# Kernel optimization log

Measured on AMD Instinct MI355X. Metric: run time of the kernel, lower is better.

Reference implementation:

```python
import jax, jax.numpy as jnp
import numpy as np

B, S, H = 4, 1024, 2048      # batch, seq_len, hidden_size
N, D = 16, 128               # num_attention_heads, attention_head_size (num_kv_heads == N)
W_SCALE = 0.02


def setup_inputs() -> dict:
    key = jax.random.key(0)
    ks = jax.random.split(key, 7)
    hidden_states = jax.random.normal(ks[0], (B, S, H), dtype=jnp.float32)
    # Per-head query projections (stacked over the head axis) + shared K/V projections.
    Wq = jax.random.normal(ks[1], (N, H, D), dtype=jnp.float32) * W_SCALE
    bq = jax.random.normal(ks[2], (N, D), dtype=jnp.float32) * W_SCALE
    Wk = jax.random.normal(ks[3], (H, D), dtype=jnp.float32) * W_SCALE
    bk = jax.random.normal(ks[4], (D,), dtype=jnp.float32) * W_SCALE
    Wv = jax.random.normal(ks[5], (H, D), dtype=jnp.float32) * W_SCALE
    bv = jax.random.normal(ks[6], (D,), dtype=jnp.float32) * W_SCALE
    return {"hidden_states": hidden_states, "Wq": Wq, "bq": bq,
            "Wk": Wk, "bk": bk, "Wv": Wv, "bv": bv}


def reference(hidden_states, Wq, bq, Wk, bk, Wv, bv):
    # Batched equivalent of the per-head Python loop:
    # q_i = Linear_i(h); k = key_layer(h); v = value_layer(h) (shared across heads,
    # repeat_interleave is a no-op since num_kv_heads == num_attention_heads).
    Q = jnp.einsum('bsh,nhd->bnsd', hidden_states, Wq) + bq[None, :, None, :]  # [B,N,S,D]
    K = hidden_states @ Wk + bk   # [B,S,D]
    V = hidden_states @ Wv + bv   # [B,S,D]
    # NOTE: source applies no 1/sqrt(D) scaling.
    scores = jnp.einsum('bnsd,btd->bnst', Q, K)          # [B,N,S,S]
    attn = jax.nn.softmax(scores, axis=-1)
    out = jnp.einsum('bnst,btd->bnsd', attn, V)          # [B,N,S,D]
    return out
```

## Files before the change

kernel.cpp:

```cpp
#include <hip/hip_runtime.h>
#include <hip/hip_bf16.h>

typedef unsigned short ushort_t;
typedef _Float16 half_t;
typedef __attribute__((ext_vector_type(8))) _Float16 h8;
typedef __attribute__((ext_vector_type(8))) short short8;
typedef __attribute__((ext_vector_type(4))) float f32x4;
typedef __attribute__((ext_vector_type(4))) float f4;

#define NB 4
#define SS 1024
#define HH 2048
#define NH 16
#define DD 128
#define MM (NB*SS)
#define NTOT 2304
#define COL_K 2048
#define COL_V 2176
#define KVB 64
#define L2E 1.44269504089f

__device__ __forceinline__ ushort_t f2h(float x) {
    half_t h = (half_t)x;
    return *(ushort_t*)&h;
}
__device__ __forceinline__ f32x4 mfma16h(h8 a, h8 b, f32x4 c) {
    return __builtin_amdgcn_mfma_f32_16x16x32_f16(a, b, c, 0, 0, 0);
}
__device__ __forceinline__ void load_lds16(const ushort_t* g, ushort_t* l) {
    __builtin_amdgcn_global_load_lds(
        (const __attribute__((address_space(1))) unsigned int*)g,
        (__attribute__((address_space(3))) unsigned int*)l,
        16, 0, 0);
}

__global__ void k_cvt(const float* __restrict__ src, ushort_t* __restrict__ dst, int n) {
    int i = (blockIdx.x * blockDim.x + threadIdx.x) * 8;
    if (i + 7 < n) {
        f4 a = *(const f4*)(src + i);
        f4 b = *(const f4*)(src + i + 4);
        short8 o;
        #pragma unroll
        for (int j = 0; j < 4; ++j) { o[j] = (short)f2h(a[j]); o[4 + j] = (short)f2h(b[j]); }
        *(short8*)(dst + i) = o;
    }
}

__global__ __launch_bounds__(256) void k_tw(const float* __restrict__ W,
                                            ushort_t* __restrict__ T, int Dd) {
    __shared__ ushort_t t[64][74];
    const int n = blockIdx.z;
    const int h0 = blockIdx.x * 64, d0 = blockIdx.y * 64;
    const int r = threadIdx.x >> 2, cg = (threadIdx.x & 3) * 16;
    const float* src = W + ((size_t)n * HH + h0 + r) * Dd + d0 + cg;
    #pragma unroll
    for (int v = 0; v < 4; ++v) {
        f4 a = *(const f4*)(src + v * 4);
        #pragma unroll
        for (int j = 0; j < 4; ++j) t[r][cg + v * 4 + j] = f2h(a[j]);
    }
    __syncthreads();
    short8 o0, o1;
    #pragma unroll
    for (int j = 0; j < 8; ++j) { o0[j] = (short)t[cg + j][r]; o1[j] = (short)t[cg + 8 + j][r]; }
    ushort_t* dst = T + ((size_t)(n * Dd + d0 + r)) * HH + h0 + cg;
    *(short8*)dst = o0;
    *(short8*)(dst + 8) = o1;
}

__global__ void k_bias(const float* __restrict__ bq, const float* __restrict__ bk,
                       const float* __restrict__ bv, float* __restrict__ bc) {
    int i = blockIdx.x * 256 + threadIdx.x;
    if (i < NTOT)
        bc[i] = (i < COL_K) ? bq[i] : ((i < COL_V) ? bk[i - COL_K] : bv[i - COL_V]);
}

__global__ __launch_bounds__(256) void k_gemm(
    const ushort_t* __restrict__ A, const ushort_t* __restrict__ B,
    const float* __restrict__ bias, ushort_t* __restrict__ O) {

    constexpr int BK = 32;
    __shared__ ushort_t sA[128 * BK], sB[128 * BK];

    const int bid = blockIdx.x;
    const int swz = (bid & 7) * 72 + (bid >> 3);
    const int m0 = (swz & 31) * 128;
    const int n0 = (swz >> 5) * 128;

    const int tid = threadIdx.x;
    const int w = tid >> 6, l = tid & 63;
    const int wr = w >> 1, wc = w & 1;
    f32x4 acc[4][4] = {};

    for (int kt = 0; kt < HH / BK; ++kt) {
        const int k0 = kt * BK;
        #pragma unroll
        for (int c = 0; c < 2; ++c) {
            int chunk = c * 4 + w;
            int idx = chunk * 512 + l * 8;
            int row = idx >> 5, kc = idx & 31;
            load_lds16(A + (size_t)(m0 + row) * HH + k0 + kc, &sA[chunk * 512]);
            load_lds16(B + (size_t)(n0 + row) * HH + k0 + kc, &sB[chunk * 512]);
        }
        __syncthreads();

        h8 a[4], b[4];
        #pragma unroll
        for (int i = 0; i < 4; ++i) {
            int ra = wr * 64 + i * 16 + (l & 15);
            int rb = wc * 64 + i * 16 + (l & 15);
            a[i] = *(const h8*)&sA[ra * 32 + (l >> 4) * 8];
            b[i] = *(const h8*)&sB[rb * 32 + (l >> 4) * 8];
        }
        #pragma unroll
        for (int i = 0; i < 4; ++i)
            #pragma unroll
            for (int j = 0; j < 4; ++j)
                acc[i][j] = mfma16h(a[i], b[j], acc[i][j]);
        __syncthreads();
    }

    #pragma unroll
    for (int i = 0; i < 4; ++i) {
        int row = m0 + wr * 64 + i * 16 + ((l >> 4) << 2);
        #pragma unroll
        for (int j = 0; j < 4; ++j) {
            int col = n0 + wc * 64 + j * 16 + (l & 15);
            float bv = bias[col];
            #pragma unroll
            for (int r = 0; r < 4; ++r) {
                float cv = acc[i][j][r] + bv;
                O[(size_t)(row + r) * NTOT + col] = f2h(cv);
            }
        }
    }
}

__global__ __launch_bounds__(256) void k_transpose_v(const ushort_t* __restrict__ O,
                                                     ushort_t* __restrict__ Vt) {
    __shared__ ushort_t t[64][74];
    const int tid = threadIdx.x;
    const int bx = blockIdx.x;
    const int by = blockIdx.y;
    int r = tid >> 2, cg = (tid & 3) * 16;
    const ushort_t* src = &O[(size_t)(bx * 64 + r) * NTOT + COL_V + by * 64 + cg];
    short8 v0 = *(const short8*)src;
    short8 v1 = *(const short8*)(src + 8);
    #pragma unroll
    for (int j = 0; j < 8; ++j) { t[r][cg + j] = (ushort_t)v0[j]; t[r][cg + 8 + j] = (ushort_t)v1[j]; }
    __syncthreads();
    short8 o0, o1;
    #pragma unroll
    for (int j = 0; j < 8; ++j) { o0[j] = (short)t[cg + j][r]; o1[j] = (short)t[cg + 8 + j][r]; }
    ushort_t* dst = &Vt[(size_t)(by * 64 + r) * MM + bx * 64 + cg];
    *(short8*)dst = o0;
    *(short8*)(dst + 8) = o1;
}

__global__ __launch_bounds__(512, 4) void k_attn(
    const ushort_t* __restrict__ O, const ushort_t* __restrict__ Vt,
    float* __restrict__ Out) {

    __shared__ ushort_t sK[2][KVB * 128];
    __shared__ ushort_t sVt[2][128 * KVB];

    const int tid = threadIdx.x;
    const int w = tid >> 6, l = tid & 63;
    const int lg = l >> 4, li = l & 15;
    const int q0 = blockIdx.x * 128;
    const int n = blockIdx.y, b = blockIdx.z;

    h8 qv[4];
    {
        size_t base = ((size_t)(b * SS + q0 + w * 16 + li)) * NTOT + n * 128 + lg * 8;
        #pragma unroll
        for (int kk = 0; kk < 4; ++kk)
            qv[kk] = *(const h8*)&O[base + kk * 32];
    }

    f32x4 accO[8] = {};
    float m2 = -3.0e38f;
    float lsum = 0.f;

    auto stage = [&](int bi, int t0) {
        #pragma unroll
        for (int c = 0; c < 2; ++c) {
            int seg = c * 8 + w;
            int oe = seg * 512 + l * 8;
            int row = oe >> 7;
            int mk = (row & 3) | (((row >> 3) & 1) << 2);
            int ce = (oe & 127) ^ (mk << 3);
            size_t g = (size_t)(b * SS + t0 + row) * NTOT + COL_K + ce;
            load_lds16(O + g, &sK[bi][seg * 512]);
        }
        #pragma unroll
        for (int c = 0; c < 2; ++c) {
            int seg = c * 8 + w;
            int oe = seg * 512 + l * 8;
            int row = oe >> 6;
            int ce = (oe & 63) ^ ((row & 7) << 3);
            size_t g = (size_t)row * MM + b * SS + t0 + ce;
            load_lds16(Vt + g, &sVt[bi][seg * 512]);
        }
    };

    stage(0, 0);
    constexpr int NT = SS / KVB;

    for (int it = 0; it < NT; ++it) {
        const int cur = it & 1;
        __syncthreads();
        if (it + 1 < NT) stage(cur ^ 1, (it + 1) * KVB);
        const ushort_t* sKc = sK[cur];
        const ushort_t* sVc = sVt[cur];

        f32x4 s[4] = {};
        #pragma unroll
        for (int ts = 0; ts < 4; ++ts) {
            int trow = (ts & 1) * 32 + ((li >> 2) << 3) + ((ts >> 1) << 2) + (li & 3);
            int mk = (trow & 3) | (((trow >> 3) & 1) << 2);
            #pragma unroll
            for (int kk = 0; kk < 4; ++kk) {
                h8 kv = *(const h8*)&sKc[trow * 128 + ((kk * 32 + lg * 8) ^ (mk << 3))];
                s[ts] = mfma16h(kv, qv[kk], s[ts]);
            }
        }

        float v = fmaxf(fmaxf(s[0][0], s[0][1]), fmaxf(s[0][2], s[0][3]));
        #pragma unroll
        for (int ts = 1; ts < 4; ++ts)
            v = fmaxf(v, fmaxf(fmaxf(s[ts][0], s[ts][1]), fmaxf(s[ts][2], s[ts][3])));
        v = fmaxf(v, __shfl_xor(v, 16));
        v = fmaxf(v, __shfl_xor(v, 32));
        float pm2 = v * L2E;

        if (!__all(pm2 <= m2 + 11.54f)) {
            float mn = fmaxf(m2, pm2);
            float scl = exp2f(m2 - mn);
            lsum *= scl;
            #pragma unroll
            for (int db = 0; db < 8; ++db)
                #pragma unroll
                for (int r = 0; r < 4; ++r) accO[db][r] *= scl;
            m2 = mn;
        }

        h8 pb[2];
        #pragma unroll
        for (int ts = 0; ts < 4; ++ts)
            #pragma unroll
            for (int r = 0; r < 4; ++r) {
                float p = exp2f(fmaf(s[ts][r], L2E, -m2));
                lsum += p;
                pb[ts & 1][((ts >> 1) << 2) + r] = (half_t)p;
            }

        #pragma unroll
        for (int db = 0; db < 8; ++db) {
            int d = db * 16 + li;
            const ushort_t* vbase = &sVc[d * KVB];
            int sw = (d & 7) << 3;
            #pragma unroll
            for (int ks = 0; ks < 2; ++ks) {
                h8 va = *(const h8*)&vbase[(ks * 32 + lg * 8) ^ sw];
                accO[db] = mfma16h(va, pb[ks], accO[db]);
            }
        }
    }

    lsum += __shfl_xor(lsum, 16);
    lsum += __shfl_xor(lsum, 32);
    float inv = 1.0f / lsum;
    int q = q0 + w * 16 + li;
    size_t base = (((size_t)b * NH + n) * SS + q) * DD;
    #pragma unroll
    for (int db = 0; db < 8; ++db) {
        f4 o;
        #pragma unroll
        for (int r = 0; r < 4; ++r) o[r] = accO[db][r] * inv;
        *(f4*)&Out[base + db * 16 + lg * 4] = o;
    }
}

#define OFF_HC    ((size_t)0)
#define OFF_BC    (OFF_HC + (size_t)MM*HH*2)
#define OFF_BIAS  (OFF_BC + (size_t)NTOT*HH*2)
#define OFF_O     (OFF_BIAS + (size_t)16384)
#define OFF_VT    (OFF_O + (size_t)MM*NTOT*2)

extern "C" void kernel_launch(void* const* d_in, const int* in_sizes, int n_in,
                              void* d_out, int out_size, void* d_ws, size_t ws_size,
                              hipStream_t stream) {
    const float* hs = (const float*)d_in[0];
    const float* Wq = (const float*)d_in[1];
    const float* bq = (const float*)d_in[2];
    const float* Wk = (const float*)d_in[3];
    const float* bk = (const float*)d_in[4];
    const float* Wv = (const float*)d_in[5];
    const float* bv = (const float*)d_in[6];
    float* out = (float*)d_out;
    char* ws = (char*)d_ws;

    ushort_t* hc   = (ushort_t*)(ws + OFF_HC);
    ushort_t* bcat = (ushort_t*)(ws + OFF_BC);
    float*    bias = (float*)(ws + OFF_BIAS);
    ushort_t* Obuf = (ushort_t*)(ws + OFF_O);
    ushort_t* vt   = (ushort_t*)(ws + OFF_VT);

    k_cvt<<<(MM*HH)/(256*8), 256, 0, stream>>>(hs, hc, MM*HH);
    dim3 gwq(HH/64, DD/64, NH);
    k_tw<<<gwq, 256, 0, stream>>>(Wq, bcat, DD);
    dim3 gwk(HH/64, DD/64, 1);
    k_tw<<<gwk, 256, 0, stream>>>(Wk, bcat + (size_t)COL_K*HH, DD);
    k_tw<<<gwk, 256, 0, stream>>>(Wv, bcat + (size_t)COL_V*HH, DD);
    k_bias<<<(NTOT + 255)/256, 256, 0, stream>>>(bq, bk, bv, bias);

    k_gemm<<<(MM/128)*(NTOT/128), 256, 0, stream>>>(hc, bcat, bias, Obuf);

    dim3 gt(MM/64, DD/64);
    k_transpose_v<<<gt, 256, 0, stream>>>(Obuf, vt);

    dim3 ga(SS/128, NH, NB);
    k_attn<<<ga, 512, 0, stream>>>(Obuf, vt, out);
}
```

Before: 133.8 us.

## Read V directly from global in attention, drop bias kernel, add setprio

The attention kernel stops staging V^T tiles into shared memory and instead loads V fragments directly from global memory (relying on cache) in the PV MFMA loop, halving LDS use per block. The separate bias concatenation kernel is removed, with the GEMM epilogue selecting bias from bq/bk/bv directly. It also adds s_setprio around MFMA sections. The direct global loads are not prefetched, so their latency may stall the PV loop, in exchange for less LDS traffic and potentially higher occupancy.

```diff
diff --git a/kernel.cpp b/kernel.cpp
--- a/kernel.cpp
+++ b/kernel.cpp
@@ -68,16 +68,10 @@
     *(short8*)(dst + 8) = o1;
 }
 
-__global__ void k_bias(const float* __restrict__ bq, const float* __restrict__ bk,
-                       const float* __restrict__ bv, float* __restrict__ bc) {
-    int i = blockIdx.x * 256 + threadIdx.x;
-    if (i < NTOT)
-        bc[i] = (i < COL_K) ? bq[i] : ((i < COL_V) ? bk[i - COL_K] : bv[i - COL_V]);
-}
-
 __global__ __launch_bounds__(256) void k_gemm(
     const ushort_t* __restrict__ A, const ushort_t* __restrict__ B,
-    const float* __restrict__ bias, ushort_t* __restrict__ O) {
+    const float* __restrict__ bq, const float* __restrict__ bk,
+    const float* __restrict__ bvv, ushort_t* __restrict__ O) {
 
     constexpr int BK = 32;
     __shared__ ushort_t sA[128 * BK], sB[128 * BK];
@@ -126,7 +120,9 @@
         #pragma unroll
         for (int j = 0; j < 4; ++j) {
             int col = n0 + wc * 64 + j * 16 + (l & 15);
-            float bv = bias[col];
+            float bv = (col < COL_K) ? bq[col]
+                     : (col < COL_V) ? bk[col - COL_K]
+                                     : bvv[col - COL_V];
             #pragma unroll
             for (int r = 0; r < 4; ++r) {
                 float cv = acc[i][j][r] + bv;
@@ -162,7 +158,6 @@
     float* __restrict__ Out) {
 
     __shared__ ushort_t sK[2][KVB * 128];
-    __shared__ ushort_t sVt[2][128 * KVB];
 
     const int tid = threadIdx.x;
     const int w = tid >> 6, l = tid & 63;
@@ -193,28 +188,21 @@
             size_t g = (size_t)(b * SS + t0 + row) * NTOT + COL_K + ce;
             load_lds16(O + g, &sK[bi][seg * 512]);
         }
-        #pragma unroll
-        for (int c = 0; c < 2; ++c) {
-            int seg = c * 8 + w;
-            int oe = seg * 512 + l * 8;
-            int row = oe >> 6;
-            int ce = (oe & 63) ^ ((row & 7) << 3);
-            size_t g = (size_t)row * MM + b * SS + t0 + ce;
-            load_lds16(Vt + g, &sVt[bi][seg * 512]);
-        }
     };
 
     stage(0, 0);
     constexpr int NT = SS / KVB;
+    const ushort_t* vtb = Vt + (size_t)b * SS;
 
     for (int it = 0; it < NT; ++it) {
         const int cur = it & 1;
+        const int t0 = it * KVB;
         __syncthreads();
-        if (it + 1 < NT) stage(cur ^ 1, (it + 1) * KVB);
+        if (it + 1 < NT) stage(cur ^ 1, t0 + KVB);
         const ushort_t* sKc = sK[cur];
-        const ushort_t* sVc = sVt[cur];
 
         f32x4 s[4] = {};
+        __builtin_amdgcn_s_setprio(1);
         #pragma unroll
         for (int ts = 0; ts < 4; ++ts) {
             int trow = (ts & 1) * 32 + ((li >> 2) << 3) + ((ts >> 1) << 2) + (li & 3);
@@ -225,6 +213,7 @@
                 s[ts] = mfma16h(kv, qv[kk], s[ts]);
             }
         }
+        __builtin_amdgcn_s_setprio(0);
 
         float v = fmaxf(fmaxf(s[0][0], s[0][1]), fmaxf(s[0][2], s[0][3]));
         #pragma unroll
@@ -255,17 +244,18 @@
                 pb[ts & 1][((ts >> 1) << 2) + r] = (half_t)p;
             }
 
+        __builtin_amdgcn_s_setprio(1);
         #pragma unroll
         for (int db = 0; db < 8; ++db) {
             int d = db * 16 + li;
-            const ushort_t* vbase = &sVc[d * KVB];
-            int sw = (d & 7) << 3;
+            const ushort_t* vrow = vtb + (size_t)d * MM + t0;
             #pragma unroll
             for (int ks = 0; ks < 2; ++ks) {
-                h8 va = *(const h8*)&vbase[(ks * 32 + lg * 8) ^ sw];
+                h8 va = *(const h8*)&vrow[ks * 32 + lg * 8];
                 accO[db] = mfma16h(va, pb[ks], accO[db]);
             }
         }
+        __builtin_amdgcn_s_setprio(0);
     }
 
     lsum += __shfl_xor(lsum, 16);
@@ -284,8 +274,7 @@
 
 #define OFF_HC    ((size_t)0)
 #define OFF_BC    (OFF_HC + (size_t)MM*HH*2)
-#define OFF_BIAS  (OFF_BC + (size_t)NTOT*HH*2)
-#define OFF_O     (OFF_BIAS + (size_t)16384)
+#define OFF_O     (OFF_BC + (size_t)NTOT*HH*2)
 #define OFF_VT    (OFF_O + (size_t)MM*NTOT*2)
 
 extern "C" void kernel_launch(void* const* d_in, const int* in_sizes, int n_in,
@@ -303,7 +292,6 @@
 
     ushort_t* hc   = (ushort_t*)(ws + OFF_HC);
     ushort_t* bcat = (ushort_t*)(ws + OFF_BC);
-    float*    bias = (float*)(ws + OFF_BIAS);
     ushort_t* Obuf = (ushort_t*)(ws + OFF_O);
     ushort_t* vt   = (ushort_t*)(ws + OFF_VT);
 
@@ -313,9 +301,8 @@
     dim3 gwk(HH/64, DD/64, 1);
     k_tw<<<gwk, 256, 0, stream>>>(Wk, bcat + (size_t)COL_K*HH, DD);
     k_tw<<<gwk, 256, 0, stream>>>(Wv, bcat + (size_t)COL_V*HH, DD);
-    k_bias<<<(NTOT + 255)/256, 256, 0, stream>>>(bq, bk, bv, bias);
-
-    k_gemm<<<(MM/128)*(NTOT/128), 256, 0, stream>>>(hc, bcat, bias, Obuf);
+
+    k_gemm<<<(MM/128)*(NTOT/128), 256, 0, stream>>>(hc, bcat, bq, bk, bv, Obuf);
 
     dim3 gt(MM/64, DD/64);
     k_transpose_v<<<gt, 256, 0, stream>>>(Obuf, vt);
```

Measured after the change: 215.4 us. 1.61x slower.
